# Performance work log

Measured on AMD Instinct MI355X. Metric: run time of the kernel, lower is better.

Reference implementation:

```python
import jax, jax.numpy as jnp
import numpy as np

B, F, Q, CHUNK = 2, 8192, 4096, 512
NUM_VERTS = 6000


def _safe_div(n, d):
    return n / jnp.where(d == 0, 1.0, d)


def _bary(a, b, c, p):
    """Barycentric coords of the closest point on triangle (a,b,c) to p.
    All args broadcastable [..., 3]; returns [..., 3] (u, v, w) with
    closest = u*a + v*b + w*c. Ericson, Real-Time Collision Detection."""
    ab = b - a; ac = c - a; ap = p - a
    d1 = jnp.sum(ab * ap, -1); d2 = jnp.sum(ac * ap, -1)
    bp = p - b
    d3 = jnp.sum(ab * bp, -1); d4 = jnp.sum(ac * bp, -1)
    cp_ = p - c
    d5 = jnp.sum(ab * cp_, -1); d6 = jnp.sum(ac * cp_, -1)
    vc = d1 * d4 - d3 * d2
    vb = d5 * d2 - d1 * d6
    va = d3 * d6 - d5 * d4
    v_ab = _safe_div(d1, d1 - d3)
    w_ac = _safe_div(d2, d2 - d6)
    w_bc = _safe_div(d4 - d3, (d4 - d3) + (d5 - d6))
    inv = _safe_div(1.0, va + vb + vc)
    v_in = vb * inv; w_in = vc * inv
    zero = jnp.zeros_like(d1); one = jnp.ones_like(d1)
    conds = [(d1 <= 0) & (d2 <= 0),
             (d3 >= 0) & (d4 <= d3),
             (vc <= 0) & (d1 >= 0) & (d3 <= 0),
             (d6 >= 0) & (d5 <= d6),
             (vb <= 0) & (d2 >= 0) & (d6 <= 0),
             (va <= 0) & (d4 >= d3) & (d5 >= d6)]
    u = jnp.select(conds, [one, zero, 1 - v_ab, zero, 1 - w_ac, zero], 1 - v_in - w_in)
    v = jnp.select(conds, [zero, one, v_ab, zero, zero, 1 - w_bc], v_in)
    w = jnp.select(conds, [zero, zero, zero, one, w_ac, w_bc], w_in)
    return jnp.stack([u, v, w], -1)


def _closest_faces(triangles, points, chunk=CHUNK):
    """Exact closest-triangle index per query point (replaces BVH search).
    triangles [B,F,3,3], points [B,Q,3] -> int32 [B,Q]."""
    tri = jax.lax.stop_gradient(triangles)
    pts = jax.lax.stop_gradient(points)
    bsz, nq = pts.shape[0], pts.shape[1]
    a = tri[:, :, 0]; b = tri[:, :, 1]; c = tri[:, :, 2]  # [B,F,3]

    def one_chunk(p_chunk):  # [B,CH,3]
        pa = p_chunk[:, :, None, :]                       # [B,CH,1,3]
        bc = _bary(a[:, None], b[:, None], c[:, None], pa)  # [B,CH,F,3]
        cp = (bc[..., 0:1] * a[:, None] + bc[..., 1:2] * b[:, None]
              + bc[..., 2:3] * c[:, None])                # [B,CH,F,3]
        d2 = jnp.sum((cp - pa) ** 2, -1)                  # [B,CH,F]
        return jnp.argmin(d2, axis=-1)                    # [B,CH]

    chunks = jnp.moveaxis(pts.reshape(bsz, nq // chunk, chunk, 3), 1, 0)
    idx = jax.lax.map(one_chunk, chunks)                  # [NC,B,CH]
    return jnp.moveaxis(idx, 0, 1).reshape(bsz, nq)


def setup_inputs() -> dict:
    key = jax.random.key(0)
    k1, k2, k3, k4, k5 = jax.random.split(key, 5)
    return {
        'triangles': jax.random.normal(k1, (B, F, 3, 3), dtype=jnp.float32),
        'points': jax.random.normal(k2, (B, Q, 3), dtype=jnp.float32),
        'normals': jax.random.normal(k3, (B, F, 3, 3), dtype=jnp.float32),
        'cmaps': jax.random.normal(k4, (B, F, 3, 3), dtype=jnp.float32),
        'faces': jax.random.randint(k5, (B, F, 3), 0, NUM_VERTS, dtype=jnp.int32),
    }


def reference(triangles, points, normals, cmaps, faces):
    closest_faces = _closest_faces(triangles, points)     # [B,Q]
    idx = closest_faces[:, :, None, None]
    tri_g = jnp.take_along_axis(triangles, idx, axis=1)   # [B,Q,3,3]
    nrm_g = jnp.take_along_axis(normals, idx, axis=1)
    cmp_g = jnp.take_along_axis(cmaps, idx, axis=1)
    bcs = _bary(tri_g[:, :, 0], tri_g[:, :, 1], tri_g[:, :, 2], points)  # [B,Q,3]
    bcs = jnp.clip(bcs, 0.0, 1.0)
    closest_points = jnp.einsum('bqk,bqkd->bqd', bcs, tri_g)
    closest_normals = jnp.einsum('bqk,bqkd->bqd', bcs, nrm_g)
    closest_cmaps = jnp.einsum('bqk,bqkd->bqd', bcs, cmp_g)
    residual = closest_points - points
    closest_fids = jnp.take_along_axis(faces, closest_faces[:, :, None], axis=1)  # [B,Q,3]
    closest_idx = jnp.take_along_axis(
        closest_fids, jnp.argmax(bcs, -1)[:, :, None], axis=2)[..., 0]            # [B,Q]
    return residual, closest_normals, closest_cmaps, closest_idx
```

## Files before the change

kernel.cpp:

```cpp
#include <hip/hip_runtime.h>
#include <float.h>

#define B_   2
#define F_   8192
#define Q_   4096
#define NC   128
#define FC   (F_/NC)
#define PTS  256
#define PPT  4

typedef float f2 __attribute__((ext_vector_type(2)));
typedef float f4u __attribute__((ext_vector_type(4), aligned(4)));
typedef unsigned int uint;

__device__ __forceinline__ f2 clamp01(f2 x) {
    f2 z = {0.f, 0.f}, o = {1.f, 1.f};
    return __builtin_elementwise_min(__builtin_elementwise_max(x, z), o);
}

__device__ __forceinline__ void bary_uvw(
    float ax, float ay, float az,
    float bx, float by, float bz,
    float cx, float cy, float cz,
    float px, float py, float pz,
    float& u, float& v, float& w)
{
#pragma clang fp contract(off)
    float abx = bx - ax, aby = by - ay, abz = bz - az;
    float acx = cx - ax, acy = cy - ay, acz = cz - az;
    float apx = px - ax, apy = py - ay, apz = pz - az;
    float d1 = abx*apx + aby*apy + abz*apz;
    float d2 = acx*apx + acy*apy + acz*apz;
    float bpx = px - bx, bpy = py - by, bpz = pz - bz;
    float d3 = abx*bpx + aby*bpy + abz*bpz;
    float d4 = acx*bpx + acy*bpy + acz*bpz;
    float qx = px - cx, qy = py - cy, qz = pz - cz;
    float d5 = abx*qx + aby*qy + abz*qz;
    float d6 = acx*qx + acy*qy + acz*qz;
    float vc = d1*d4 - d3*d2;
    float vb = d5*d2 - d1*d6;
    float va = d3*d6 - d5*d4;

    bool c1 = (d1 <= 0.f) && (d2 <= 0.f);
    bool c2 = (d3 >= 0.f) && (d4 <= d3);
    bool c3 = (vc <= 0.f) && (d1 >= 0.f) && (d3 <= 0.f);
    bool c4 = (d6 >= 0.f) && (d5 <= d6);
    bool c5 = (vb <= 0.f) && (d2 >= 0.f) && (d6 <= 0.f);
    bool c6 = (va <= 0.f) && (d4 >= d3) && (d5 >= d6);

    bool e1 = c1;
    bool p1 = !c1;
    bool e2 = p1 && c2;
    bool p2 = p1 && !c2;
    bool e3 = p2 && c3;
    bool p3 = p2 && !c3;
    bool e4 = p3 && c4;
    bool p4 = p3 && !c4;
    bool e5 = p4 && c5;
    bool p5 = p4 && !c5;
    bool e6 = p5 && c6;

    float d43 = d4 - d3;
    float d56 = d5 - d6;
    float n  = e3 ? d1        : (e5 ? d2        : (e6 ? d43         : 1.f));
    float dd = e3 ? (d1 - d3) : (e5 ? (d2 - d6) : (e6 ? (d43 + d56) : (va + vb + vc)));
    dd = (dd == 0.f) ? 1.f : dd;
    float t = n / dd;

    float vi = vb * t;
    float wi = vc * t;
    u = e1 ? 1.f : (e2 ? 0.f : (e3 ? 1.f - t : (e4 ? 0.f : (e5 ? 1.f - t : (e6 ? 0.f     : 1.f - vi - wi)))));
    v = e1 ? 0.f : (e2 ? 1.f : (e3 ? t       : (e4 ? 0.f : (e5 ? 0.f     : (e6 ? 1.f - t : vi)))));
    w = e1 ? 0.f : (e2 ? 0.f : (e3 ? 0.f     : (e4 ? 1.f : (e5 ? t       : (e6 ? t       : wi)))));
}

__device__ __forceinline__ f2 pair_dist(
    f2 px, f2 py, f2 pz,
    float ax, float ay, float az,
    float abx, float aby, float abz,
    float acx, float acy, float acz,
    float daa, float dcc, float dac, float dbc, float kk,
    float rdaa, float rdcc, float rdbc, float rnn)
{
    f2 apx = px - ax, apy = py - ay, apz = pz - az;
    f2 d1  = abx*apx + aby*apy + abz*apz;
    f2 d2  = acx*apx + acy*apy + acz*apz;
    f2 app = apx*apx + apy*apy + apz*apz;

    f2 t1 = d1*dcc - d2*dac;
    f2 t2 = d2*daa - d1*dac;
    f2 t12n = 1.f - (t1 + t2)*rnn;
    f2 sgr  = (d1*t1 + d2*t2)*rnn;
    f2 ins  = __builtin_elementwise_min(__builtin_elementwise_min(t1, t2), t12n);

    f2 td1 = d1 + d1;
    f2 tab = clamp01(d1 * rdaa);
    f2 rab = tab*(td1 - tab*daa);
    f2 tac = clamp01(d2 * rdcc);
    f2 rac = tac*((d2 + d2) - tac*dcc);
    f2 d43 = (d2 - d1) + kk;
    f2 sbc = clamp01(d43 * rdbc);
    f2 rbc = (td1 - daa) + sbc*((d43 + d43) - sbc*dbc);
    f2 rmax = __builtin_elementwise_max(__builtin_elementwise_max(rab, rac), rbc);

    f2 red;
    red.x = (ins.x >= 0.f) ? sgr.x : rmax.x;
    red.y = (ins.y >= 0.f) ? sgr.y : rmax.y;
    f2 z = {0.f, 0.f};
    return __builtin_elementwise_max(app - red, z);
}

__global__ __launch_bounds__(PTS, 4) void scan_kernel(
    const float* __restrict__ tri, const float* __restrict__ pts,
    uint2* __restrict__ keys)
{
    __shared__ float4 S[FC * 6];
    const int tid = threadIdx.x;
    const int pb = blockIdx.x, cb = blockIdx.y, bb = blockIdx.z;

    if (tid < FC) {
        const float* g = tri + ((size_t)bb * F_ + (size_t)cb * FC + tid) * 9;
        float ax = g[0], ay = g[1], az = g[2];
        float bx = g[3], by = g[4], bz = g[5];
        float cx = g[6], cy = g[7], cz = g[8];
        float abx = bx - ax, aby = by - ay, abz = bz - az;
        float acx = cx - ax, acy = cy - ay, acz = cz - az;
        float daa = abx*abx + aby*aby + abz*abz;
        float dcc = acx*acx + acy*acy + acz*acz;
        float dac = abx*acx + aby*acy + abz*acz;
        float dbc = daa + dcc - 2.f*dac;
        float nn  = daa*dcc - dac*dac;
        S[tid*6 + 0] = make_float4(ax, ay, az, daa);
        S[tid*6 + 1] = make_float4(abx, aby, abz, dcc);
        S[tid*6 + 2] = make_float4(acx, acy, acz, dac);
        S[tid*6 + 3] = make_float4(1.f/daa, 1.f/dcc, 1.f/dbc, 1.f/nn);
        S[tid*6 + 4] = make_float4(bx, by, bz, 0.f);
        S[tid*6 + 5] = make_float4(cx, cy, cz, 0.f);
    }
    __syncthreads();

    const int q0 = pb * (PTS * PPT) + tid * PPT;
    const float* p0 = pts + ((size_t)bb * Q_ + q0) * 3;
    f4u l0 = *(const f4u*)(p0);
    f4u l1 = *(const f4u*)(p0 + 4);
    f4u l2 = *(const f4u*)(p0 + 8);
    f2 pxA = {l0.x, l0.w}, pyA = {l0.y, l1.x}, pzA = {l0.z, l1.y};
    f2 pxB = {l1.z, l2.y}, pyB = {l1.w, l2.z}, pzB = {l2.x, l2.w};

    uint k00 = 0xFFFFFFFFu, k01 = 0xFFFFFFFFu;
    uint k10 = 0xFFFFFFFFu, k11 = 0xFFFFFFFFu;
    uint k20 = 0xFFFFFFFFu, k21 = 0xFFFFFFFFu;
    uint k30 = 0xFFFFFFFFu, k31 = 0xFFFFFFFFu;
    #pragma unroll 2
    for (int fl = 0; fl < FC; ++fl) {
        float4 c0 = S[fl*6 + 0];
        float4 c1 = S[fl*6 + 1];
        float4 c2 = S[fl*6 + 2];
        float4 c3 = S[fl*6 + 3];
        float daa = c0.w, dcc = c1.w, dac = c2.w;
        float dbc = daa + dcc - 2.f*dac;
        float kk  = daa - dac;

        f2 dA = pair_dist(pxA, pyA, pzA, c0.x, c0.y, c0.z,
                          c1.x, c1.y, c1.z, c2.x, c2.y, c2.z,
                          daa, dcc, dac, dbc, kk, c3.x, c3.y, c3.z, c3.w);
        f2 dB = pair_dist(pxB, pyB, pzB, c0.x, c0.y, c0.z,
                          c1.x, c1.y, c1.z, c2.x, c2.y, c2.z,
                          daa, dcc, dac, dbc, kk, c3.x, c3.y, c3.z, c3.w);

        uint kA0 = (__float_as_uint(dA.x) & 0xFFFFFFC0u) | (uint)fl;
        uint kA1 = (__float_as_uint(dA.y) & 0xFFFFFFC0u) | (uint)fl;
        uint kB0 = (__float_as_uint(dB.x) & 0xFFFFFFC0u) | (uint)fl;
        uint kB1 = (__float_as_uint(dB.y) & 0xFFFFFFC0u) | (uint)fl;
        uint lo, hi;
        lo = min(k00, kA0); hi = max(k00, kA0); k00 = lo; k01 = min(k01, hi);
        lo = min(k10, kA1); hi = max(k10, kA1); k10 = lo; k11 = min(k11, hi);
        lo = min(k20, kB0); hi = max(k20, kB0); k20 = lo; k21 = min(k21, hi);
        lo = min(k30, kB1); hi = max(k30, kB1); k30 = lo; k31 = min(k31, hi);
    }

    float pxs[4] = {l0.x, l0.w, l1.z, l2.y};
    float pys[4] = {l0.y, l1.x, l1.w, l2.z};
    float pzs[4] = {l0.z, l1.y, l2.x, l2.w};
    uint kk0[4] = {k00, k10, k20, k30};
    uint kk1[4] = {k01, k11, k21, k31};

    #pragma unroll
    for (int p = 0; p < 4; ++p) {
        float px = pxs[p], py = pys[p], pz = pzs[p];
        float dbest = FLT_MAX; int fbest = 0x7FFFFFFF;
        #pragma unroll
        for (int j = 0; j < 2; ++j) {
            int lf = (int)((j == 0 ? kk0[p] : kk1[p]) & 63u);
            float4 ra = S[lf*6 + 0];
            float4 rb = S[lf*6 + 4];
            float4 rc = S[lf*6 + 5];
            float u, v, w;
            bary_uvw(ra.x, ra.y, ra.z, rb.x, rb.y, rb.z, rc.x, rc.y, rc.z,
                     px, py, pz, u, v, w);
            float d2v;
            {
#pragma clang fp contract(off)
                float cpx = u*ra.x + v*rb.x + w*rc.x;
                float cpy = u*ra.y + v*rb.y + w*rc.y;
                float cpz = u*ra.z + v*rb.z + w*rc.z;
                float dx = cpx - px, dy = cpy - py, dz = cpz - pz;
                d2v = dx*dx + dy*dy + dz*dz;
            }
            int face = cb * FC + lf;
            if (d2v < dbest || (d2v == dbest && face < fbest)) { dbest = d2v; fbest = face; }
        }
        keys[((size_t)bb * Q_ + q0 + p) * NC + cb] = make_uint2(__float_as_uint(dbest), (uint)fbest);
    }
}

__global__ __launch_bounds__(256) void finalize_kernel(
    const float* __restrict__ tri, const float* __restrict__ pts,
    const float* __restrict__ nrm, const float* __restrict__ cmp,
    const int* __restrict__ faces,
    const uint2* __restrict__ keys,
    float* __restrict__ out)
{
#pragma clang fp contract(off)
    const int lane = threadIdx.x & 63;
    const int t = blockIdx.x * 4 + (threadIdx.x >> 6);
    const int bb = t >> 12;

    uint4 K = ((const uint4*)keys)[(size_t)t * (NC/2) + lane];
    float dbest = __uint_as_float(K.x); int fbest = (int)K.y;
    float d1v   = __uint_as_float(K.z); int f1v   = (int)K.w;
    if (d1v < dbest || (d1v == dbest && f1v < fbest)) { dbest = d1v; fbest = f1v; }
    for (int off = 32; off > 0; off >>= 1) {
        float od = __shfl_down(dbest, off);
        int   of = __shfl_down(fbest, off);
        if (od < dbest || (od == dbest && of < fbest)) { dbest = od; fbest = of; }
    }
    if (lane != 0) return;

    const float* pp = pts + (size_t)t * 3;
    float px = pp[0], py = pp[1], pz = pp[2];

    const int bestf = fbest;
    const float* tg = tri + ((size_t)bb * F_ + bestf) * 9;
    const float* ng = nrm + ((size_t)bb * F_ + bestf) * 9;
    const float* cg = cmp + ((size_t)bb * F_ + bestf) * 9;
    f4u TA = *(const f4u*)(tg), TB = *(const f4u*)(tg + 4);
    float TC = tg[8];
    f4u NA = *(const f4u*)(ng), NB = *(const f4u*)(ng + 4);
    float NCs = ng[8];
    f4u CA = *(const f4u*)(cg), CB = *(const f4u*)(cg + 4);
    float CC = cg[8];

    float u, v, w;
    bary_uvw(TA.x, TA.y, TA.z, TA.w, TB.x, TB.y, TB.z, TB.w, TC,
             px, py, pz, u, v, w);
    u = fminf(fmaxf(u, 0.f), 1.f);
    v = fminf(fmaxf(v, 0.f), 1.f);
    w = fminf(fmaxf(w, 0.f), 1.f);

    float cpx = u * TA.x + v * TA.w + w * TB.z;
    float cpy = u * TA.y + v * TB.x + w * TB.w;
    float cpz = u * TA.z + v * TB.y + w * TC;
    float nx  = u * NA.x + v * NA.w + w * NB.z;
    float ny  = u * NA.y + v * NB.x + w * NB.w;
    float nz  = u * NA.z + v * NB.y + w * NCs;
    float mx  = u * CA.x + v * CA.w + w * CB.z;
    float my  = u * CA.y + v * CB.x + w * CB.w;
    float mz  = u * CA.z + v * CB.y + w * CC;

    const size_t S3 = (size_t)B_ * Q_ * 3;
    out[(size_t)t * 3 + 0] = cpx - px;
    out[(size_t)t * 3 + 1] = cpy - py;
    out[(size_t)t * 3 + 2] = cpz - pz;
    out[S3 + (size_t)t * 3 + 0] = nx;
    out[S3 + (size_t)t * 3 + 1] = ny;
    out[S3 + (size_t)t * 3 + 2] = nz;
    out[2 * S3 + (size_t)t * 3 + 0] = mx;
    out[2 * S3 + (size_t)t * 3 + 1] = my;
    out[2 * S3 + (size_t)t * 3 + 2] = mz;

    int k = 0; float mm = u;
    if (v > mm) { mm = v; k = 1; }
    if (w > mm) { k = 2; }
    out[3 * S3 + t] = (float)faces[((size_t)bb * F_ + bestf) * 3 + k];
}

extern "C" void kernel_launch(void* const* d_in, const int* in_sizes, int n_in,
                              void* d_out, int out_size, void* d_ws, size_t ws_size,
                              hipStream_t stream) {
    const float* tri   = (const float*)d_in[0];
    const float* pts   = (const float*)d_in[1];
    const float* nrm   = (const float*)d_in[2];
    const float* cmp   = (const float*)d_in[3];
    const int*   faces = (const int*)d_in[4];
    float* out = (float*)d_out;

    uint2* keys = (uint2*)d_ws;

    dim3 g1(Q_ / (PTS * PPT), NC, B_);
    scan_kernel<<<g1, PTS, 0, stream>>>(tri, pts, keys);
    finalize_kernel<<<(B_ * Q_) / 4, 256, 0, stream>>>(
        tri, pts, nrm, cmp, faces, keys, out);
}
```

Baseline: 141.8 us.

## Template scan over face-chunk size, use 256 chunks and drop distance clamp

Templates the scan and finalize kernels on the face-chunk size. When the workspace allows, it uses 32-face chunks split into 256 chunks, which doubles the grid and the candidate keys, and finalize then reduces four keys per lane instead of two. It also raises launch bounds to 8 blocks per SIMD, switches the packed keys to signed ints, and drops the max-with-zero clamp on the approximate distance, so small negative values now sort correctly as signed. The cost is more keys to write and read and a larger workspace, in exchange for more parallelism and shorter per-block loops.

```diff
diff --git a/kernel.cpp b/kernel.cpp
--- a/kernel.cpp
+++ b/kernel.cpp
@@ -4,8 +4,6 @@
 #define B_   2
 #define F_   8192
 #define Q_   4096
-#define NC   128
-#define FC   (F_/NC)
 #define PTS  256
 #define PPT  4
 
@@ -106,20 +104,22 @@
     f2 red;
     red.x = (ins.x >= 0.f) ? sgr.x : rmax.x;
     red.y = (ins.y >= 0.f) ? sgr.y : rmax.y;
-    f2 z = {0.f, 0.f};
-    return __builtin_elementwise_max(app - red, z);
-}
-
-__global__ __launch_bounds__(PTS, 4) void scan_kernel(
+    return app - red;
+}
+
+template<int FCv>
+__global__ __launch_bounds__(PTS, 8) void scan_kernel(
     const float* __restrict__ tri, const float* __restrict__ pts,
     uint2* __restrict__ keys)
 {
-    __shared__ float4 S[FC * 6];
+    constexpr int NCv = F_ / FCv;
+    constexpr int IM  = ~(FCv - 1);
+    __shared__ float4 S[FCv * 6];
     const int tid = threadIdx.x;
     const int pb = blockIdx.x, cb = blockIdx.y, bb = blockIdx.z;
 
-    if (tid < FC) {
-        const float* g = tri + ((size_t)bb * F_ + (size_t)cb * FC + tid) * 9;
+    if (tid < FCv) {
+        const float* g = tri + ((size_t)bb * F_ + (size_t)cb * FCv + tid) * 9;
         float ax = g[0], ay = g[1], az = g[2];
         float bx = g[3], by = g[4], bz = g[5];
         float cx = g[6], cy = g[7], cz = g[8];
@@ -147,12 +147,12 @@
     f2 pxA = {l0.x, l0.w}, pyA = {l0.y, l1.x}, pzA = {l0.z, l1.y};
     f2 pxB = {l1.z, l2.y}, pyB = {l1.w, l2.z}, pzB = {l2.x, l2.w};
 
-    uint k00 = 0xFFFFFFFFu, k01 = 0xFFFFFFFFu;
-    uint k10 = 0xFFFFFFFFu, k11 = 0xFFFFFFFFu;
-    uint k20 = 0xFFFFFFFFu, k21 = 0xFFFFFFFFu;
-    uint k30 = 0xFFFFFFFFu, k31 = 0xFFFFFFFFu;
+    int k00 = 0x7FFFFFFF, k01 = 0x7FFFFFFF;
+    int k10 = 0x7FFFFFFF, k11 = 0x7FFFFFFF;
+    int k20 = 0x7FFFFFFF, k21 = 0x7FFFFFFF;
+    int k30 = 0x7FFFFFFF, k31 = 0x7FFFFFFF;
     #pragma unroll 2
-    for (int fl = 0; fl < FC; ++fl) {
+    for (int fl = 0; fl < FCv; ++fl) {
         float4 c0 = S[fl*6 + 0];
         float4 c1 = S[fl*6 + 1];
         float4 c2 = S[fl*6 + 2];
@@ -168,11 +168,11 @@
                           c1.x, c1.y, c1.z, c2.x, c2.y, c2.z,
                           daa, dcc, dac, dbc, kk, c3.x, c3.y, c3.z, c3.w);
 
-        uint kA0 = (__float_as_uint(dA.x) & 0xFFFFFFC0u) | (uint)fl;
-        uint kA1 = (__float_as_uint(dA.y) & 0xFFFFFFC0u) | (uint)fl;
-        uint kB0 = (__float_as_uint(dB.x) & 0xFFFFFFC0u) | (uint)fl;
-        uint kB1 = (__float_as_uint(dB.y) & 0xFFFFFFC0u) | (uint)fl;
-        uint lo, hi;
+        int kA0 = (__float_as_int(dA.x) & IM) | fl;
+        int kA1 = (__float_as_int(dA.y) & IM) | fl;
+        int kB0 = (__float_as_int(dB.x) & IM) | fl;
+        int kB1 = (__float_as_int(dB.y) & IM) | fl;
+        int lo, hi;
         lo = min(k00, kA0); hi = max(k00, kA0); k00 = lo; k01 = min(k01, hi);
         lo = min(k10, kA1); hi = max(k10, kA1); k10 = lo; k11 = min(k11, hi);
         lo = min(k20, kB0); hi = max(k20, kB0); k20 = lo; k21 = min(k21, hi);
@@ -182,8 +182,8 @@
     float pxs[4] = {l0.x, l0.w, l1.z, l2.y};
     float pys[4] = {l0.y, l1.x, l1.w, l2.z};
     float pzs[4] = {l0.z, l1.y, l2.x, l2.w};
-    uint kk0[4] = {k00, k10, k20, k30};
-    uint kk1[4] = {k01, k11, k21, k31};
+    int kk0[4] = {k00, k10, k20, k30};
+    int kk1[4] = {k01, k11, k21, k31};
 
     #pragma unroll
     for (int p = 0; p < 4; ++p) {
@@ -191,7 +191,7 @@
         float dbest = FLT_MAX; int fbest = 0x7FFFFFFF;
         #pragma unroll
         for (int j = 0; j < 2; ++j) {
-            int lf = (int)((j == 0 ? kk0[p] : kk1[p]) & 63u);
+            int lf = (j == 0 ? kk0[p] : kk1[p]) & (FCv - 1);
             float4 ra = S[lf*6 + 0];
             float4 rb = S[lf*6 + 4];
             float4 rc = S[lf*6 + 5];
@@ -207,13 +207,14 @@
                 float dx = cpx - px, dy = cpy - py, dz = cpz - pz;
                 d2v = dx*dx + dy*dy + dz*dz;
             }
-            int face = cb * FC + lf;
+            int face = cb * FCv + lf;
             if (d2v < dbest || (d2v == dbest && face < fbest)) { dbest = d2v; fbest = face; }
         }
-        keys[((size_t)bb * Q_ + q0 + p) * NC + cb] = make_uint2(__float_as_uint(dbest), (uint)fbest);
-    }
-}
-
+        keys[((size_t)bb * Q_ + q0 + p) * NCv + cb] = make_uint2(__float_as_uint(dbest), (uint)fbest);
+    }
+}
+
+template<int NCv>
 __global__ __launch_bounds__(256) void finalize_kernel(
     const float* __restrict__ tri, const float* __restrict__ pts,
     const float* __restrict__ nrm, const float* __restrict__ cmp,
@@ -226,10 +227,18 @@
     const int t = blockIdx.x * 4 + (threadIdx.x >> 6);
     const int bb = t >> 12;
 
-    uint4 K = ((const uint4*)keys)[(size_t)t * (NC/2) + lane];
+    const uint4* kp = (const uint4*)keys + (size_t)t * (NCv/2);
+    uint4 K = kp[lane];
     float dbest = __uint_as_float(K.x); int fbest = (int)K.y;
     float d1v   = __uint_as_float(K.z); int f1v   = (int)K.w;
     if (d1v < dbest || (d1v == dbest && f1v < fbest)) { dbest = d1v; fbest = f1v; }
+    if (NCv == 256) {
+        uint4 K2 = kp[lane + 64];
+        float d2v = __uint_as_float(K2.x); int f2v = (int)K2.y;
+        if (d2v < dbest || (d2v == dbest && f2v < fbest)) { dbest = d2v; fbest = f2v; }
+        float d3v = __uint_as_float(K2.z); int f3v = (int)K2.w;
+        if (d3v < dbest || (d3v == dbest && f3v < fbest)) { dbest = d3v; fbest = f3v; }
+    }
     for (int off = 32; off > 0; off >>= 1) {
         float od = __shfl_down(dbest, off);
         int   of = __shfl_down(fbest, off);
@@ -297,8 +306,16 @@
 
     uint2* keys = (uint2*)d_ws;
 
-    dim3 g1(Q_ / (PTS * PPT), NC, B_);
-    scan_kernel<<<g1, PTS, 0, stream>>>(tri, pts, keys);
-    finalize_kernel<<<(B_ * Q_) / 4, 256, 0, stream>>>(
-        tri, pts, nrm, cmp, faces, keys, out);
-}
+    const size_t need256 = (size_t)B_ * Q_ * 256 * sizeof(uint2);
+    if (ws_size >= need256) {
+        dim3 g1(Q_ / (PTS * PPT), 256, B_);
+        scan_kernel<32><<<g1, PTS, 0, stream>>>(tri, pts, keys);
+        finalize_kernel<256><<<(B_ * Q_) / 4, 256, 0, stream>>>(
+            tri, pts, nrm, cmp, faces, keys, out);
+    } else {
+        dim3 g1(Q_ / (PTS * PPT), 128, B_);
+        scan_kernel<64><<<g1, PTS, 0, stream>>>(tri, pts, keys);
+        finalize_kernel<128><<<(B_ * Q_) / 4, 256, 0, stream>>>(
+            tri, pts, nrm, cmp, faces, keys, out);
+    }
+}
```

Result: slower. 154.9 us (+9.2%).

## Pack two triangles per packed-FP32 lane and precompute negated constants in LDS

Applied to the files above, without the earlier changes.

Reorganizes the inner distance scan so each packed f2 operation evaluates one point against two triangles, instead of two points against one triangle. Triangle constants, including negated and derived terms, are stored interleaved in LDS so the loop can use explicit v_pk_fma/v_pk_mul/v_pk_add inline asm and avoid scalar-to-vector broadcasts and separate subtractions. Top-2 key maintenance now merges a sorted pair per step. The final clamp to zero is dropped, so slightly negative distances may produce odd sign-bit keys. Inline asm also limits what the compiler can schedule.

```diff
diff --git a/kernel.cpp b/kernel.cpp
--- a/kernel.cpp
+++ b/kernel.cpp
@@ -12,6 +12,16 @@
 typedef float f2 __attribute__((ext_vector_type(2)));
 typedef float f4u __attribute__((ext_vector_type(4), aligned(4)));
 typedef unsigned int uint;
+
+__device__ __forceinline__ f2 pk_fma(f2 a, f2 b, f2 c) {
+    f2 d; asm("v_pk_fma_f32 %0, %1, %2, %3" : "=v"(d) : "v"(a), "v"(b), "v"(c)); return d;
+}
+__device__ __forceinline__ f2 pk_mul(f2 a, f2 b) {
+    f2 d; asm("v_pk_mul_f32 %0, %1, %2" : "=v"(d) : "v"(a), "v"(b)); return d;
+}
+__device__ __forceinline__ f2 pk_add(f2 a, f2 b) {
+    f2 d; asm("v_pk_add_f32 %0, %1, %2" : "=v"(d) : "v"(a), "v"(b)); return d;
+}
 
 __device__ __forceinline__ f2 clamp01(f2 x) {
     f2 z = {0.f, 0.f}, o = {1.f, 1.f};
@@ -74,47 +84,52 @@
     w = e1 ? 0.f : (e2 ? 0.f : (e3 ? 0.f     : (e4 ? 1.f : (e5 ? t       : (e6 ? t       : wi)))));
 }
 
-__device__ __forceinline__ f2 pair_dist(
+__device__ __forceinline__ f2 tri_pair_dist(
     f2 px, f2 py, f2 pz,
-    float ax, float ay, float az,
-    float abx, float aby, float abz,
-    float acx, float acy, float acz,
-    float daa, float dcc, float dac, float dbc, float kk,
-    float rdaa, float rdcc, float rdbc, float rnn)
+    f2 nax, f2 nay, f2 naz,
+    f2 abx, f2 aby, f2 abz,
+    f2 acx, f2 acy, f2 acz,
+    f2 daa, f2 dcc, f2 ndac,
+    f2 ndaa, f2 ndcc, f2 ndbc,
+    f2 kk,  f2 rdaa, f2 rdcc, f2 rdbc, f2 rnn, f2 nn, f2 NEG1)
 {
-    f2 apx = px - ax, apy = py - ay, apz = pz - az;
-    f2 d1  = abx*apx + aby*apy + abz*apz;
-    f2 d2  = acx*apx + acy*apy + acz*apz;
-    f2 app = apx*apx + apy*apy + apz*apz;
-
-    f2 t1 = d1*dcc - d2*dac;
-    f2 t2 = d2*daa - d1*dac;
-    f2 t12n = 1.f - (t1 + t2)*rnn;
-    f2 sgr  = (d1*t1 + d2*t2)*rnn;
-    f2 ins  = __builtin_elementwise_min(__builtin_elementwise_min(t1, t2), t12n);
-
-    f2 td1 = d1 + d1;
-    f2 tab = clamp01(d1 * rdaa);
-    f2 rab = tab*(td1 - tab*daa);
-    f2 tac = clamp01(d2 * rdcc);
-    f2 rac = tac*((d2 + d2) - tac*dcc);
-    f2 d43 = (d2 - d1) + kk;
-    f2 sbc = clamp01(d43 * rdbc);
-    f2 rbc = (td1 - daa) + sbc*((d43 + d43) - sbc*dbc);
+    f2 apx = pk_add(px, nax), apy = pk_add(py, nay), apz = pk_add(pz, naz);
+    f2 d1  = pk_fma(abz, apz, pk_fma(aby, apy, pk_mul(abx, apx)));
+    f2 d2  = pk_fma(acz, apz, pk_fma(acy, apy, pk_mul(acx, apx)));
+    f2 app = pk_fma(apz, apz, pk_fma(apy, apy, pk_mul(apx, apx)));
+
+    f2 t1  = pk_fma(d1, dcc, pk_mul(d2, ndac));
+    f2 t2  = pk_fma(d2, daa, pk_mul(d1, ndac));
+    f2 s12 = pk_add(t1, t2);
+    f2 t12n = pk_fma(s12, NEG1, nn);
+    f2 sgr = pk_mul(pk_fma(d2, t2, pk_mul(d1, t1)), rnn);
+    f2 ins = __builtin_elementwise_min(__builtin_elementwise_min(t1, t2), t12n);
+
+    f2 td1 = pk_add(d1, d1);
+    f2 tab = clamp01(pk_mul(d1, rdaa));
+    f2 rab = pk_mul(tab, pk_fma(tab, ndaa, td1));
+    f2 td2 = pk_add(d2, d2);
+    f2 tac = clamp01(pk_mul(d2, rdcc));
+    f2 rac = pk_mul(tac, pk_fma(tac, ndcc, td2));
+    f2 d43 = pk_add(pk_fma(d1, NEG1, d2), kk);
+    f2 sbc = clamp01(pk_mul(d43, rdbc));
+    f2 rbc = pk_add(pk_add(td1, ndaa),
+                    pk_mul(sbc, pk_fma(sbc, ndbc, pk_add(d43, d43))));
     f2 rmax = __builtin_elementwise_max(__builtin_elementwise_max(rab, rac), rbc);
 
     f2 red;
     red.x = (ins.x >= 0.f) ? sgr.x : rmax.x;
     red.y = (ins.y >= 0.f) ? sgr.y : rmax.y;
-    f2 z = {0.f, 0.f};
-    return __builtin_elementwise_max(app - red, z);
+    return pk_fma(red, NEG1, app);
 }
 
 __global__ __launch_bounds__(PTS, 4) void scan_kernel(
     const float* __restrict__ tri, const float* __restrict__ pts,
     uint2* __restrict__ keys)
 {
-    __shared__ float4 S[FC * 6];
+    constexpr int IM = ~(FC - 1);
+    __shared__ float4 SP4[(FC/2) * 11];
+    __shared__ float4 SR[FC * 3];
     const int tid = threadIdx.x;
     const int pb = blockIdx.x, cb = blockIdx.y, bb = blockIdx.z;
 
@@ -130,12 +145,18 @@
         float dac = abx*acx + aby*acy + abz*acz;
         float dbc = daa + dcc - 2.f*dac;
         float nn  = daa*dcc - dac*dac;
-        S[tid*6 + 0] = make_float4(ax, ay, az, daa);
-        S[tid*6 + 1] = make_float4(abx, aby, abz, dcc);
-        S[tid*6 + 2] = make_float4(acx, acy, acz, dac);
-        S[tid*6 + 3] = make_float4(1.f/daa, 1.f/dcc, 1.f/dbc, 1.f/nn);
-        S[tid*6 + 4] = make_float4(bx, by, bz, 0.f);
-        S[tid*6 + 5] = make_float4(cx, cy, cz, 0.f);
+        float* w = (float*)SP4 + (tid >> 1) * 44 + (tid & 1);
+        w[0]  = -ax;      w[2]  = -ay;      w[4]  = -az;
+        w[6]  = abx;      w[8]  = aby;      w[10] = abz;
+        w[12] = acx;      w[14] = acy;      w[16] = acz;
+        w[18] = daa;      w[20] = dcc;      w[22] = -dac;
+        w[24] = -daa;     w[26] = -dcc;     w[28] = -dbc;
+        w[30] = daa - dac;
+        w[32] = 1.f/daa;  w[34] = 1.f/dcc;  w[36] = 1.f/dbc;
+        w[38] = 1.f/nn;   w[40] = nn;       w[42] = 0.f;
+        SR[tid*3 + 0] = make_float4(ax, ay, az, 0.f);
+        SR[tid*3 + 1] = make_float4(bx, by, bz, 0.f);
+        SR[tid*3 + 2] = make_float4(cx, cy, cz, 0.f);
     }
     __syncthreads();
 
@@ -144,46 +165,53 @@
     f4u l0 = *(const f4u*)(p0);
     f4u l1 = *(const f4u*)(p0 + 4);
     f4u l2 = *(const f4u*)(p0 + 8);
-    f2 pxA = {l0.x, l0.w}, pyA = {l0.y, l1.x}, pzA = {l0.z, l1.y};
-    f2 pxB = {l1.z, l2.y}, pyB = {l1.w, l2.z}, pzB = {l2.x, l2.w};
-
-    uint k00 = 0xFFFFFFFFu, k01 = 0xFFFFFFFFu;
-    uint k10 = 0xFFFFFFFFu, k11 = 0xFFFFFFFFu;
-    uint k20 = 0xFFFFFFFFu, k21 = 0xFFFFFFFFu;
-    uint k30 = 0xFFFFFFFFu, k31 = 0xFFFFFFFFu;
-    #pragma unroll 2
-    for (int fl = 0; fl < FC; ++fl) {
-        float4 c0 = S[fl*6 + 0];
-        float4 c1 = S[fl*6 + 1];
-        float4 c2 = S[fl*6 + 2];
-        float4 c3 = S[fl*6 + 3];
-        float daa = c0.w, dcc = c1.w, dac = c2.w;
-        float dbc = daa + dcc - 2.f*dac;
-        float kk  = daa - dac;
-
-        f2 dA = pair_dist(pxA, pyA, pzA, c0.x, c0.y, c0.z,
-                          c1.x, c1.y, c1.z, c2.x, c2.y, c2.z,
-                          daa, dcc, dac, dbc, kk, c3.x, c3.y, c3.z, c3.w);
-        f2 dB = pair_dist(pxB, pyB, pzB, c0.x, c0.y, c0.z,
-                          c1.x, c1.y, c1.z, c2.x, c2.y, c2.z,
-                          daa, dcc, dac, dbc, kk, c3.x, c3.y, c3.z, c3.w);
-
-        uint kA0 = (__float_as_uint(dA.x) & 0xFFFFFFC0u) | (uint)fl;
-        uint kA1 = (__float_as_uint(dA.y) & 0xFFFFFFC0u) | (uint)fl;
-        uint kB0 = (__float_as_uint(dB.x) & 0xFFFFFFC0u) | (uint)fl;
-        uint kB1 = (__float_as_uint(dB.y) & 0xFFFFFFC0u) | (uint)fl;
-        uint lo, hi;
-        lo = min(k00, kA0); hi = max(k00, kA0); k00 = lo; k01 = min(k01, hi);
-        lo = min(k10, kA1); hi = max(k10, kA1); k10 = lo; k11 = min(k11, hi);
-        lo = min(k20, kB0); hi = max(k20, kB0); k20 = lo; k21 = min(k21, hi);
-        lo = min(k30, kB1); hi = max(k30, kB1); k30 = lo; k31 = min(k31, hi);
-    }
-
     float pxs[4] = {l0.x, l0.w, l1.z, l2.y};
     float pys[4] = {l0.y, l1.x, l1.w, l2.z};
     float pzs[4] = {l0.z, l1.y, l2.x, l2.w};
-    uint kk0[4] = {k00, k10, k20, k30};
-    uint kk1[4] = {k01, k11, k21, k31};
+
+    f2 PX[4], PY[4], PZ[4];
+    #pragma unroll
+    for (int p = 0; p < 4; ++p) {
+        PX[p].x = pxs[p]; PX[p].y = pxs[p];
+        PY[p].x = pys[p]; PY[p].y = pys[p];
+        PZ[p].x = pzs[p]; PZ[p].y = pzs[p];
+    }
+    f2 NEG1 = {-1.f, -1.f};
+
+    int K0[4] = {0x7FFFFFFF, 0x7FFFFFFF, 0x7FFFFFFF, 0x7FFFFFFF};
+    int K1[4] = {0x7FFFFFFF, 0x7FFFFFFF, 0x7FFFFFFF, 0x7FFFFFFF};
+
+    for (int j = 0; j < FC/2; ++j) {
+        const float4* r = SP4 + j * 11;
+        float4 F0 = r[0], F1 = r[1], F2v = r[2], F3 = r[3], F4v = r[4];
+        float4 F5 = r[5], F6 = r[6], F7 = r[7], F8 = r[8], F9 = r[9];
+        float4 F10 = r[10];
+        f2 nax = {F0.x, F0.y},  nay = {F0.z, F0.w};
+        f2 naz = {F1.x, F1.y},  abx = {F1.z, F1.w};
+        f2 aby = {F2v.x, F2v.y}, abz = {F2v.z, F2v.w};
+        f2 acx = {F3.x, F3.y},  acy = {F3.z, F3.w};
+        f2 acz = {F4v.x, F4v.y}, daa = {F4v.z, F4v.w};
+        f2 dcc = {F5.x, F5.y},  ndac = {F5.z, F5.w};
+        f2 ndaa = {F6.x, F6.y}, ndcc = {F6.z, F6.w};
+        f2 ndbc = {F7.x, F7.y}, kk = {F7.z, F7.w};
+        f2 rdaa = {F8.x, F8.y}, rdcc = {F8.z, F8.w};
+        f2 rdbc = {F9.x, F9.y}, rnn = {F9.z, F9.w};
+        f2 nn  = {F10.x, F10.y};
+
+        #pragma unroll
+        for (int p = 0; p < 4; ++p) {
+            f2 d = tri_pair_dist(PX[p], PY[p], PZ[p],
+                                 nax, nay, naz, abx, aby, abz, acx, acy, acz,
+                                 daa, dcc, ndac, ndaa, ndcc, ndbc,
+                                 kk, rdaa, rdcc, rdbc, rnn, nn, NEG1);
+            int kx = (__float_as_int(d.x) & IM) | (2*j);
+            int ky = (__float_as_int(d.y) & IM) | (2*j + 1);
+            int lo = min(kx, ky), hi = max(kx, ky);
+            int m  = max(K0[p], lo);
+            K0[p] = min(K0[p], lo);
+            K1[p] = min(min(K1[p], hi), m);
+        }
+    }
 
     #pragma unroll
     for (int p = 0; p < 4; ++p) {
@@ -191,10 +219,10 @@
         float dbest = FLT_MAX; int fbest = 0x7FFFFFFF;
         #pragma unroll
         for (int j = 0; j < 2; ++j) {
-            int lf = (int)((j == 0 ? kk0[p] : kk1[p]) & 63u);
-            float4 ra = S[lf*6 + 0];
-            float4 rb = S[lf*6 + 4];
-            float4 rc = S[lf*6 + 5];
+            int lf = (j == 0 ? K0[p] : K1[p]) & (FC - 1);
+            float4 ra = SR[lf*3 + 0];
+            float4 rb = SR[lf*3 + 1];
+            float4 rc = SR[lf*3 + 2];
             float u, v, w;
             bary_uvw(ra.x, ra.y, ra.z, rb.x, rb.y, rb.z, rc.x, rc.y, rc.z,
                      px, py, pz, u, v, w);
```

Result: faster. 138.2 us (-2.6%).

## Precompute plane-offset coefficients and scalarize per-point triangle distance scan

Applied to the files above, without the earlier changes.

Rewrites the inner distance scan to use precomputed affine coefficients, so d1, d2 and |p-a|^2 each come from one fma chain per point. It drops the packed float2 pair_dist helper in favour of a scalar loop over four points. It changes the inside test to compare against nn rather than a normalized 1 - t*rnn, and replaces unsigned keys with signed int keys without clamping the distance to zero. The shared layout is split into a scan table and a refinement table. This cuts ALU ops per point-triangle pair, but loses packed-FP32 pairing and changes rounding and sign handling of negative distances, which may affect candidate selection.

```diff
diff --git a/kernel.cpp b/kernel.cpp
--- a/kernel.cpp
+++ b/kernel.cpp
@@ -9,13 +9,11 @@
 #define PTS  256
 #define PPT  4
 
-typedef float f2 __attribute__((ext_vector_type(2)));
 typedef float f4u __attribute__((ext_vector_type(4), aligned(4)));
 typedef unsigned int uint;
 
-__device__ __forceinline__ f2 clamp01(f2 x) {
-    f2 z = {0.f, 0.f}, o = {1.f, 1.f};
-    return __builtin_elementwise_min(__builtin_elementwise_max(x, z), o);
+__device__ __forceinline__ float clamp01s(float x) {
+    return fminf(fmaxf(x, 0.f), 1.f);
 }
 
 __device__ __forceinline__ void bary_uvw(
@@ -74,47 +72,13 @@
     w = e1 ? 0.f : (e2 ? 0.f : (e3 ? 0.f     : (e4 ? 1.f : (e5 ? t       : (e6 ? t       : wi)))));
 }
 
-__device__ __forceinline__ f2 pair_dist(
-    f2 px, f2 py, f2 pz,
-    float ax, float ay, float az,
-    float abx, float aby, float abz,
-    float acx, float acy, float acz,
-    float daa, float dcc, float dac, float dbc, float kk,
-    float rdaa, float rdcc, float rdbc, float rnn)
-{
-    f2 apx = px - ax, apy = py - ay, apz = pz - az;
-    f2 d1  = abx*apx + aby*apy + abz*apz;
-    f2 d2  = acx*apx + acy*apy + acz*apz;
-    f2 app = apx*apx + apy*apy + apz*apz;
-
-    f2 t1 = d1*dcc - d2*dac;
-    f2 t2 = d2*daa - d1*dac;
-    f2 t12n = 1.f - (t1 + t2)*rnn;
-    f2 sgr  = (d1*t1 + d2*t2)*rnn;
-    f2 ins  = __builtin_elementwise_min(__builtin_elementwise_min(t1, t2), t12n);
-
-    f2 td1 = d1 + d1;
-    f2 tab = clamp01(d1 * rdaa);
-    f2 rab = tab*(td1 - tab*daa);
-    f2 tac = clamp01(d2 * rdcc);
-    f2 rac = tac*((d2 + d2) - tac*dcc);
-    f2 d43 = (d2 - d1) + kk;
-    f2 sbc = clamp01(d43 * rdbc);
-    f2 rbc = (td1 - daa) + sbc*((d43 + d43) - sbc*dbc);
-    f2 rmax = __builtin_elementwise_max(__builtin_elementwise_max(rab, rac), rbc);
-
-    f2 red;
-    red.x = (ins.x >= 0.f) ? sgr.x : rmax.x;
-    red.y = (ins.y >= 0.f) ? sgr.y : rmax.y;
-    f2 z = {0.f, 0.f};
-    return __builtin_elementwise_max(app - red, z);
-}
-
 __global__ __launch_bounds__(PTS, 4) void scan_kernel(
     const float* __restrict__ tri, const float* __restrict__ pts,
     uint2* __restrict__ keys)
 {
-    __shared__ float4 S[FC * 6];
+    constexpr int IM = ~(FC - 1);
+    __shared__ float4 SC[FC * 5];
+    __shared__ float4 SR[FC * 3];
     const int tid = threadIdx.x;
     const int pb = blockIdx.x, cb = blockIdx.y, bb = blockIdx.z;
 
@@ -130,12 +94,14 @@
         float dac = abx*acx + aby*acy + abz*acz;
         float dbc = daa + dcc - 2.f*dac;
         float nn  = daa*dcc - dac*dac;
-        S[tid*6 + 0] = make_float4(ax, ay, az, daa);
-        S[tid*6 + 1] = make_float4(abx, aby, abz, dcc);
-        S[tid*6 + 2] = make_float4(acx, acy, acz, dac);
-        S[tid*6 + 3] = make_float4(1.f/daa, 1.f/dcc, 1.f/dbc, 1.f/nn);
-        S[tid*6 + 4] = make_float4(bx, by, bz, 0.f);
-        S[tid*6 + 5] = make_float4(cx, cy, cz, 0.f);
+        SC[tid*5 + 0] = make_float4(abx, aby, abz, -(abx*ax + aby*ay + abz*az));
+        SC[tid*5 + 1] = make_float4(acx, acy, acz, -(acx*ax + acy*ay + acz*az));
+        SC[tid*5 + 2] = make_float4(-2.f*ax, -2.f*ay, -2.f*az, ax*ax + ay*ay + az*az);
+        SC[tid*5 + 3] = make_float4(daa, dcc, dac, nn);
+        SC[tid*5 + 4] = make_float4(1.f/daa, 1.f/dcc, 1.f/dbc, 1.f/nn);
+        SR[tid*3 + 0] = make_float4(ax, ay, az, 0.f);
+        SR[tid*3 + 1] = make_float4(bx, by, bz, 0.f);
+        SR[tid*3 + 2] = make_float4(cx, cy, cz, 0.f);
     }
     __syncthreads();
 
@@ -144,46 +110,63 @@
     f4u l0 = *(const f4u*)(p0);
     f4u l1 = *(const f4u*)(p0 + 4);
     f4u l2 = *(const f4u*)(p0 + 8);
-    f2 pxA = {l0.x, l0.w}, pyA = {l0.y, l1.x}, pzA = {l0.z, l1.y};
-    f2 pxB = {l1.z, l2.y}, pyB = {l1.w, l2.z}, pzB = {l2.x, l2.w};
-
-    uint k00 = 0xFFFFFFFFu, k01 = 0xFFFFFFFFu;
-    uint k10 = 0xFFFFFFFFu, k11 = 0xFFFFFFFFu;
-    uint k20 = 0xFFFFFFFFu, k21 = 0xFFFFFFFFu;
-    uint k30 = 0xFFFFFFFFu, k31 = 0xFFFFFFFFu;
-    #pragma unroll 2
-    for (int fl = 0; fl < FC; ++fl) {
-        float4 c0 = S[fl*6 + 0];
-        float4 c1 = S[fl*6 + 1];
-        float4 c2 = S[fl*6 + 2];
-        float4 c3 = S[fl*6 + 3];
-        float daa = c0.w, dcc = c1.w, dac = c2.w;
-        float dbc = daa + dcc - 2.f*dac;
-        float kk  = daa - dac;
-
-        f2 dA = pair_dist(pxA, pyA, pzA, c0.x, c0.y, c0.z,
-                          c1.x, c1.y, c1.z, c2.x, c2.y, c2.z,
-                          daa, dcc, dac, dbc, kk, c3.x, c3.y, c3.z, c3.w);
-        f2 dB = pair_dist(pxB, pyB, pzB, c0.x, c0.y, c0.z,
-                          c1.x, c1.y, c1.z, c2.x, c2.y, c2.z,
-                          daa, dcc, dac, dbc, kk, c3.x, c3.y, c3.z, c3.w);
-
-        uint kA0 = (__float_as_uint(dA.x) & 0xFFFFFFC0u) | (uint)fl;
-        uint kA1 = (__float_as_uint(dA.y) & 0xFFFFFFC0u) | (uint)fl;
-        uint kB0 = (__float_as_uint(dB.x) & 0xFFFFFFC0u) | (uint)fl;
-        uint kB1 = (__float_as_uint(dB.y) & 0xFFFFFFC0u) | (uint)fl;
-        uint lo, hi;
-        lo = min(k00, kA0); hi = max(k00, kA0); k00 = lo; k01 = min(k01, hi);
-        lo = min(k10, kA1); hi = max(k10, kA1); k10 = lo; k11 = min(k11, hi);
-        lo = min(k20, kB0); hi = max(k20, kB0); k20 = lo; k21 = min(k21, hi);
-        lo = min(k30, kB1); hi = max(k30, kB1); k30 = lo; k31 = min(k31, hi);
-    }
-
     float pxs[4] = {l0.x, l0.w, l1.z, l2.y};
     float pys[4] = {l0.y, l1.x, l1.w, l2.z};
     float pzs[4] = {l0.z, l1.y, l2.x, l2.w};
-    uint kk0[4] = {k00, k10, k20, k30};
-    uint kk1[4] = {k01, k11, k21, k31};
+    float pps[4];
+    #pragma unroll
+    for (int p = 0; p < 4; ++p)
+        pps[p] = pxs[p]*pxs[p] + pys[p]*pys[p] + pzs[p]*pzs[p];
+
+    int K0[4] = {0x7FFFFFFF, 0x7FFFFFFF, 0x7FFFFFFF, 0x7FFFFFFF};
+    int K1[4] = {0x7FFFFFFF, 0x7FFFFFFF, 0x7FFFFFFF, 0x7FFFFFFF};
+
+    #pragma unroll 2
+    for (int fl = 0; fl < FC; ++fl) {
+        float4 c0 = SC[fl*5 + 0];
+        float4 c1 = SC[fl*5 + 1];
+        float4 c2 = SC[fl*5 + 2];
+        float4 c3 = SC[fl*5 + 3];
+        float4 c4 = SC[fl*5 + 4];
+        float daa = c3.x, dcc = c3.y, dac = c3.z, nn = c3.w;
+        float kk  = daa - dac;
+        float dbc = daa + dcc - 2.f*dac;
+
+        #pragma unroll
+        for (int p = 0; p < 4; ++p) {
+            float px = pxs[p], py = pys[p], pz = pzs[p];
+            float d1 = fmaf(c0.x, px, fmaf(c0.y, py, fmaf(c0.z, pz, c0.w)));
+            float d2 = fmaf(c1.x, px, fmaf(c1.y, py, fmaf(c1.z, pz, c1.w)));
+            float s  = fmaf(c2.x, px, fmaf(c2.y, py, fmaf(c2.z, pz, c2.w)));
+            float app = s + pps[p];
+
+            float t1 = d1*dcc - d2*dac;
+            float t2 = d2*daa - d1*dac;
+            float ts = t1 + t2;
+            float t12n = nn - ts;
+            float ins  = fminf(fminf(t1, t2), t12n);
+            float sgr  = (d1*t1 + d2*t2) * c4.w;
+
+            float td1 = d1 + d1;
+            float tab = clamp01s(d1 * c4.x);
+            float rab = tab * (td1 - tab*daa);
+            float td2 = d2 + d2;
+            float tac = clamp01s(d2 * c4.y);
+            float rac = tac * (td2 - tac*dcc);
+            float d43 = (d2 - d1) + kk;
+            float sbc = clamp01s(d43 * c4.z);
+            float rbc = (td1 - daa) + sbc * ((d43 + d43) - sbc*dbc);
+            float rmax = fmaxf(fmaxf(rab, rac), rbc);
+
+            float red = (ins >= 0.f) ? sgr : rmax;
+            float d = app - red;
+
+            int k = (__float_as_int(d) & IM) | fl;
+            int m = max(K0[p], k);
+            K0[p] = min(K0[p], k);
+            K1[p] = min(K1[p], m);
+        }
+    }
 
     #pragma unroll
     for (int p = 0; p < 4; ++p) {
@@ -191,10 +174,10 @@
         float dbest = FLT_MAX; int fbest = 0x7FFFFFFF;
         #pragma unroll
         for (int j = 0; j < 2; ++j) {
-            int lf = (int)((j == 0 ? kk0[p] : kk1[p]) & 63u);
-            float4 ra = S[lf*6 + 0];
-            float4 rb = S[lf*6 + 4];
-            float4 rc = S[lf*6 + 5];
+            int lf = (j == 0 ? K0[p] : K1[p]) & (FC - 1);
+            float4 ra = SR[lf*3 + 0];
+            float4 rb = SR[lf*3 + 1];
+            float4 rc = SR[lf*3 + 2];
             float u, v, w;
             bary_uvw(ra.x, ra.y, ra.z, rb.x, rb.y, rb.z, rc.x, rc.y, rc.z,
                      px, py, pz, u, v, w);
```

Measured after the change: 146.3 us. +3.2%, slower.
